# Performance work log

Hardware: AMD Instinct MI355X
Metric: run time of the kernel (lower is better)

## Reference

```python
import jax, jax.numpy as jnp
import numpy as np

MAX_OOV = 50

def setup_inputs() -> dict:
    key = jax.random.key(0)
    ks = jax.random.split(key, 20)
    B, T, Tc, E, H, V = 128, 256, 200, 256, 512, 50000
    s = 0.02
    inp = {
        'input': jax.random.randint(ks[0], (B, 1), 0, V),
        'h0': jax.random.normal(ks[1], (1, B, H), jnp.float32),
        'c0': jax.random.normal(ks[2], (1, B, H), jnp.float32),
        'encoder_outputs': jax.random.normal(ks[3], (B, T, H), jnp.float32),
        'context_encoder_outputs': jax.random.normal(ks[4], (B, Tc, H), jnp.float32),
        'context_input': jax.random.randint(ks[5], (B, Tc), 0, V + MAX_OOV),
        'embedding': jax.random.normal(ks[6], (V, E), jnp.float32) * s,
        'W_ih': jax.random.normal(ks[7], (4 * H, E), jnp.float32) * s,
        'W_hh': jax.random.normal(ks[8], (4 * H, H), jnp.float32) * s,
        'b_ih': jnp.zeros((4 * H,), jnp.float32),
        'b_hh': jnp.zeros((4 * H,), jnp.float32),
        'attn_W': jax.random.normal(ks[9], (H, H), jnp.float32) * s,
        'attn_b': jnp.zeros((H,), jnp.float32),
        'cattn_W': jax.random.normal(ks[10], (H, H), jnp.float32) * s,
        'cattn_b': jnp.zeros((H,), jnp.float32),
        'gen_W': jax.random.normal(ks[11], (1, 3 * H + E), jnp.float32) * s,
        'gen_b': jnp.zeros((1,), jnp.float32),
        'sig_b': jax.random.uniform(ks[12], (1,), jnp.float32, -0.1, 0.1),
        'out_W': jax.random.normal(ks[13], (V, H), jnp.float32) * s,
        'out_b': jnp.zeros((V,), jnp.float32),
    }
    return inp

def reference(input, h0, c0, encoder_outputs, context_encoder_outputs, context_input,
              embedding, W_ih, W_hh, b_ih, b_hh, attn_W, attn_b, cattn_W, cattn_b,
              gen_W, gen_b, sig_b, out_W, out_b):
    B = input.shape[0]
    V = out_W.shape[0]
    Vext = V + MAX_OOV
    # embedding lookup (input_len == 1)
    emb = embedding[input[:, 0]]                       # [B, E]
    # single-step LSTM (PyTorch gate order: i, f, g, o)
    gates = emb @ W_ih.T + b_ih + h0[0] @ W_hh.T + b_hh  # [B, 4H]
    i, f, g, o = jnp.split(gates, 4, axis=-1)
    c1 = jax.nn.sigmoid(f) * c0[0] + jax.nn.sigmoid(i) * jnp.tanh(g)
    h1 = jax.nn.sigmoid(o) * jnp.tanh(c1)              # [B, H]
    output = h1
    # attention over encoder_outputs (context_only)
    dec = output @ attn_W.T + attn_b                   # [B, H]
    scores = jax.nn.softmax(jnp.einsum('bth,bh->bt', encoder_outputs, dec), axis=1)
    context = jnp.einsum('bt,bth->bh', scores, encoder_outputs)
    # context attention (score_only)
    cdec = output @ cattn_W.T + cattn_b
    cscores = jax.nn.softmax(jnp.einsum('bth,bh->bt', context_encoder_outputs, cdec), axis=1)  # [B, Tc]
    cctx = jnp.einsum('bt,bth->bh', cscores, context_encoder_outputs)
    # generation probability
    feats = jnp.concatenate([context, cctx, output, emb], axis=1)  # [B, 3H+E]
    p_gen = jax.nn.sigmoid(feats @ gen_W.T + gen_b + sig_b)        # [B, 1]
    ctx_len = (context_input > 0).sum(axis=1, keepdims=True)
    p_gen = jnp.where(ctx_len == 0, jnp.float32(1.0), p_gen)
    # vocab distribution, extended with oov zeros
    p_vocab = jax.nn.softmax(output @ out_W.T + out_b, axis=1)
    p_vocab = jnp.concatenate([p_vocab, jnp.zeros((B, MAX_OOV), p_vocab.dtype)], axis=1)
    # copy distribution: scatter-add attention scores into extended vocab
    p_copy = jnp.zeros((B, Vext), p_vocab.dtype).at[
        jnp.arange(B)[:, None], context_input].add(cscores)
    prob = p_gen * p_vocab + (1.0 - p_gen) * p_copy
    logp = jnp.log(jnp.clip(prob, 1e-10))
    return logp, (h1[None], c1[None])
```

## Files before the change

### kernel.cpp

```cpp
#include <hip/hip_runtime.h>
#include <hip/hip_bf16.h>

#define BB 128
#define T_ENC 256
#define T_CTX 200
#define E_DIM 256
#define H_DIM 512
#define V_DIM 50000
#define N_OOV 50
#define VEXT  50050
#define FOURH 2048
#define K_GATES 768
#define LOGP_SZ (BB * VEXT)
#define OUT_H1_OFF LOGP_SZ
#define OUT_C1_OFF (LOGP_SZ + BB * H_DIM)
#define VCHUNK 2048
#define NCHUNK 25
#define NBIG 782

typedef __bf16 bf16x8 __attribute__((ext_vector_type(8)));
typedef float  floatx4 __attribute__((ext_vector_type(4)));

__device__ __forceinline__ float wave_sum(float v) {
#pragma unroll
  for (int m = 32; m > 0; m >>= 1) v += __shfl_xor(v, m, 64);
  return v;
}

__device__ __forceinline__ float sigm(float x) { return 1.0f / (1.0f + __expf(-x)); }

__device__ __forceinline__ unsigned f2bf2(float a, float b) {
  unsigned ua = __float_as_uint(a), ub = __float_as_uint(b);
  ua = (ua + 0x7FFFu + ((ua >> 16) & 1u)) >> 16;
  ub = (ub + 0x7FFFu + ((ub >> 16) & 1u)) & 0xFFFF0000u;
  return ua | ub;
}

__global__ __launch_bounds__(256) void prep_all(
    const float* __restrict__ W_ih, const float* __restrict__ W_hh,
    const float* __restrict__ attnW, const float* __restrict__ cattnW,
    const float* __restrict__ attnb, const float* __restrict__ cattnb,
    const int* __restrict__ input, const float* __restrict__ embT,
    const float* __restrict__ h0,
    __bf16* __restrict__ Wcat, __bf16* __restrict__ Wattn, float* __restrict__ attnbc,
    __bf16* __restrict__ Abuf, float* __restrict__ embf) {
  int n = blockIdx.x, tid = threadIdx.x;
  if (n < 2048) {
    unsigned* wr = (unsigned*)(Wcat + (size_t)n * K_GATES);
    for (int idx = tid; idx < 384; idx += 256) {
      int e0 = idx * 2;
      float2 x = (e0 < 256) ? *(const float2*)(W_ih + (size_t)n * E_DIM + e0)
                            : *(const float2*)(W_hh + (size_t)n * H_DIM + e0 - 256);
      wr[idx] = f2bf2(x.x, x.y);
    }
    if (n < 1024) {
      const float* src = (n < 512) ? (attnW + (size_t)n * H_DIM) : (cattnW + (size_t)(n - 512) * H_DIM);
      unsigned* wa = (unsigned*)(Wattn + (size_t)n * H_DIM);
      float2 x = *(const float2*)(src + tid * 2);
      wa[tid] = f2bf2(x.x, x.y);
    }
    if (n < 4) {
      int i = n * 256 + tid;
      attnbc[i] = (i < 512) ? attnb[i] : cattnb[i - 512];
    }
  } else {
    int b = n - 2048;
    int tok = input[b];
    unsigned* ar = (unsigned*)(Abuf + (size_t)b * K_GATES);
    for (int idx = tid; idx < 384; idx += 256) {
      int e0 = idx * 2;
      float2 x;
      if (e0 < 256) {
        x = *(const float2*)(embT + (size_t)tok * E_DIM + e0);
        *(float2*)(embf + b * E_DIM + e0) = x;
      } else {
        x = *(const float2*)(h0 + (size_t)b * H_DIM + e0 - 256);
      }
      ar[idx] = f2bf2(x.x, x.y);
    }
  }
}

template <int BF32>
__device__ __forceinline__ void gemm64_body(
    const __bf16* __restrict__ Abf, const void* __restrict__ Bsrc,
    const float* __restrict__ bias, float* __restrict__ C,
    int n0, int N, int Koff, int Klen, int Kpitch, int ldc) {
  __shared__ __bf16 As[128][72];
  __shared__ __bf16 Bs[64][72];
  int tid = threadIdx.x, lane = tid & 63, wid = tid >> 6;

  floatx4 acc[2][4];
#pragma unroll
  for (int i = 0; i < 2; i++)
#pragma unroll
    for (int j = 0; j < 4; j++) acc[i][j] = (floatx4){0.f, 0.f, 0.f, 0.f};

  int arow = tid >> 1, ahalf = tid & 1;
  int brow = tid >> 2, bq = tid & 3;
  int gnb = n0 + brow; if (gnb > N - 1) gnb = N - 1;

  const __bf16* abase = Abf + (size_t)arow * Kpitch + Koff + ahalf * 32;
  const float*  bfb = (const float*)Bsrc + (size_t)gnb * Kpitch + Koff + bq * 16;
  const __bf16* bhb = (const __bf16*)Bsrc + (size_t)gnb * Kpitch + Koff + bq * 16;

  uint4 ra[4];
  float4 rbf[4];
  uint4 rbh[2];
  {
    const uint4* s = (const uint4*)abase;
    ra[0] = s[0]; ra[1] = s[1]; ra[2] = s[2]; ra[3] = s[3];
    if (BF32) { const float4* t = (const float4*)bfb; rbf[0] = t[0]; rbf[1] = t[1]; rbf[2] = t[2]; rbf[3] = t[3]; }
    else      { const uint4* t = (const uint4*)bhb;  rbh[0] = t[0]; rbh[1] = t[1]; }
  }

  for (int k0 = 0; k0 < Klen; k0 += 64) {
    __syncthreads();
    { uint4* d = (uint4*)&As[arow][ahalf * 32]; d[0] = ra[0]; d[1] = ra[1]; d[2] = ra[2]; d[3] = ra[3]; }
    if (BF32) {
      uint4 o0, o1;
      o0.x = f2bf2(rbf[0].x, rbf[0].y); o0.y = f2bf2(rbf[0].z, rbf[0].w);
      o0.z = f2bf2(rbf[1].x, rbf[1].y); o0.w = f2bf2(rbf[1].z, rbf[1].w);
      o1.x = f2bf2(rbf[2].x, rbf[2].y); o1.y = f2bf2(rbf[2].z, rbf[2].w);
      o1.z = f2bf2(rbf[3].x, rbf[3].y); o1.w = f2bf2(rbf[3].z, rbf[3].w);
      uint4* d = (uint4*)&Bs[brow][bq * 16]; d[0] = o0; d[1] = o1;
    } else {
      uint4* d = (uint4*)&Bs[brow][bq * 16]; d[0] = rbh[0]; d[1] = rbh[1];
    }
    if (k0 + 64 < Klen) {
      const uint4* s = (const uint4*)(abase + k0 + 64);
      ra[0] = s[0]; ra[1] = s[1]; ra[2] = s[2]; ra[3] = s[3];
      if (BF32) { const float4* t = (const float4*)(bfb + k0 + 64); rbf[0] = t[0]; rbf[1] = t[1]; rbf[2] = t[2]; rbf[3] = t[3]; }
      else      { const uint4* t = (const uint4*)(bhb + k0 + 64);  rbh[0] = t[0]; rbh[1] = t[1]; }
    }
    __syncthreads();
#pragma unroll
    for (int kk = 0; kk < 64; kk += 32) {
      int kbase = kk + (lane >> 4) * 8;
      bf16x8 a0 = *(const bf16x8*)&As[wid * 32 + (lane & 15)][kbase];
      bf16x8 a1 = *(const bf16x8*)&As[wid * 32 + 16 + (lane & 15)][kbase];
      bf16x8 bfr[4];
#pragma unroll
      for (int j = 0; j < 4; j++) bfr[j] = *(const bf16x8*)&Bs[j * 16 + (lane & 15)][kbase];
#pragma unroll
      for (int j = 0; j < 4; j++) {
        acc[0][j] = __builtin_amdgcn_mfma_f32_16x16x32_bf16(a0, bfr[j], acc[0][j], 0, 0, 0);
        acc[1][j] = __builtin_amdgcn_mfma_f32_16x16x32_bf16(a1, bfr[j], acc[1][j], 0, 0, 0);
      }
    }
  }
  int cn = lane & 15, cq = lane >> 4;
#pragma unroll
  for (int i = 0; i < 2; i++)
#pragma unroll
    for (int j = 0; j < 4; j++)
#pragma unroll
      for (int r = 0; r < 4; r++) {
        int row = wid * 32 + i * 16 + cq * 4 + r;
        int col = n0 + j * 16 + cn;
        if (col < N) {
          float v = acc[i][j][r];
          if (bias) v += bias[col];
          C[(size_t)row * ldc + col] = v;
        }
      }
}

__global__ __launch_bounds__(256) void gates_gemm(
    const __bf16* __restrict__ Abuf, const __bf16* __restrict__ Wcat,
    float* __restrict__ g0, float* __restrict__ g1) {
  int bx = blockIdx.x;
  int kh = bx >> 5, nb = bx & 31;
  gemm64_body<0>(Abuf, Wcat, nullptr, kh ? g1 : g0, nb * 64, FOURH, kh * 384, 384, K_GATES, FOURH);
}

__global__ __launch_bounds__(256) void mega_gemm(
    const __bf16* __restrict__ h1b, const float* __restrict__ outW,
    const float* __restrict__ outb, float* __restrict__ Cbig,
    const __bf16* __restrict__ Wattn, const float* __restrict__ attnbc,
    float* __restrict__ decbuf) {
  int bx = blockIdx.x;
  if (bx < NBIG) gemm64_body<1>(h1b, outW, outb, Cbig, bx * 64, V_DIM, 0, H_DIM, H_DIM, VEXT);
  else           gemm64_body<0>(h1b, Wattn, attnbc, decbuf, (bx - NBIG) * 64, 1024, 0, H_DIM, H_DIM, 1024);
}

__global__ __launch_bounds__(256) void lstm_kernel(
    const float* __restrict__ gA, const float* __restrict__ gB,
    const float* __restrict__ b_ih, const float* __restrict__ b_hh,
    const float* __restrict__ c0,
    float* __restrict__ h1_out, float* __restrict__ c1_out, __bf16* __restrict__ h1b) {
  int idx = blockIdx.x * 256 + threadIdx.x;
  int b = idx >> 9, j = idx & 511;
  const float* ga = gA + b * FOURH;
  const float* gb = gB + b * FOURH;
  float iv = ga[j]        + gb[j]        + b_ih[j]        + b_hh[j];
  float fv = ga[512 + j]  + gb[512 + j]  + b_ih[512 + j]  + b_hh[512 + j];
  float gv = ga[1024 + j] + gb[1024 + j] + b_ih[1024 + j] + b_hh[1024 + j];
  float ov = ga[1536 + j] + gb[1536 + j] + b_ih[1536 + j] + b_hh[1536 + j];
  float c1 = sigm(fv) * c0[idx] + sigm(iv) * tanhf(gv);
  float h1 = sigm(ov) * tanhf(c1);
  h1_out[idx] = h1;
  c1_out[idx] = c1;
  h1b[idx] = (__bf16)h1;
}

__device__ __forceinline__ void flash_body(
    int g, const float* __restrict__ enc, const float* __restrict__ cenc,
    const float* __restrict__ decbuf, float* __restrict__ opart,
    float2* __restrict__ mlb, float* __restrict__ rawsc) {
  __shared__ float so[4][512];
  __shared__ float sml[4][2];
  int b = g & 127;
  int cc = g >> 7;
  int which = cc >> 2, chunk = cc & 3;
  int tchunk = which ? 50 : 64;
  int t0 = chunk * tchunk;
  const float* src = which ? (cenc + (size_t)b * T_CTX * H_DIM) : (enc + (size_t)b * T_ENC * H_DIM);
  const float* decp = decbuf + b * 1024 + which * 512;
  int tid = threadIdx.x, lane = tid & 63, wid = tid >> 6;
  float4 d0 = *(const float4*)(decp + lane * 8);
  float4 d1 = *(const float4*)(decp + lane * 8 + 4);
  float m = -1e30f, l = 0.f;
  float4 o0 = {0.f, 0.f, 0.f, 0.f}, o1 = {0.f, 0.f, 0.f, 0.f};
  for (int t = t0 + wid; t < t0 + tchunk; t += 4) {
    const float* row = src + (size_t)t * H_DIM + lane * 8;
    float4 r0 = *(const float4*)row;
    float4 r1 = *(const float4*)(row + 4);
    float p = r0.x * d0.x + r0.y * d0.y + r0.z * d0.z + r0.w * d0.w +
              r1.x * d1.x + r1.y * d1.y + r1.z * d1.z + r1.w * d1.w;
    p = wave_sum(p);
    if (which && lane == 0) rawsc[b * T_CTX + t] = p;
    float mn = fmaxf(m, p);
    float sc = __expf(m - mn);
    float e  = __expf(p - mn);
    l = l * sc + e;
    o0.x = o0.x * sc + e * r0.x; o0.y = o0.y * sc + e * r0.y;
    o0.z = o0.z * sc + e * r0.z; o0.w = o0.w * sc + e * r0.w;
    o1.x = o1.x * sc + e * r1.x; o1.y = o1.y * sc + e * r1.y;
    o1.z = o1.z * sc + e * r1.z; o1.w = o1.w * sc + e * r1.w;
    m = mn;
  }
  *(float4*)&so[wid][lane * 8]     = o0;
  *(float4*)&so[wid][lane * 8 + 4] = o1;
  if (lane == 0) { sml[wid][0] = m; sml[wid][1] = l; }
  __syncthreads();
  float M = fmaxf(fmaxf(sml[0][0], sml[1][0]), fmaxf(sml[2][0], sml[3][0]));
  float w0 = __expf(sml[0][0] - M), w1 = __expf(sml[1][0] - M);
  float w2 = __expf(sml[2][0] - M), w3 = __expf(sml[3][0] - M);
  float L = w0 * sml[0][1] + w1 * sml[1][1] + w2 * sml[2][1] + w3 * sml[3][1];
  int h = tid, h2 = tid + 256;
  float O0 = w0 * so[0][h]  + w1 * so[1][h]  + w2 * so[2][h]  + w3 * so[3][h];
  float O1 = w0 * so[0][h2] + w1 * so[1][h2] + w2 * so[2][h2] + w3 * so[3][h2];
  opart[(size_t)g * 512 + h]  = O0;
  opart[(size_t)g * 512 + h2] = O1;
  if (tid == 0) mlb[g] = make_float2(M, L);
}

__device__ __forceinline__ void stats_body(
    int bx, const float* __restrict__ logits,
    float* __restrict__ mpart, float* __restrict__ spart) {
  __shared__ float sm[256], ss[256];
  int b = bx & 127, c = bx >> 7;
  int tid = threadIdx.x;
  const float* rowp = logits + (size_t)b * VEXT;
  int v0 = c * VCHUNK + tid * 8;
  float m = -1e30f, s = 0.f;
#pragma unroll
  for (int k = 0; k < 4; k++) {
    int v = v0 + 2 * k;
    float2 x = *(const float2*)(rowp + v);
    if (v < V_DIM) {
      float xv = x.x;
      if (xv > m) { s = s * __expf(m - xv) + 1.0f; m = xv; } else s += __expf(xv - m);
    }
    if (v + 1 < V_DIM) {
      float xv = x.y;
      if (xv > m) { s = s * __expf(m - xv) + 1.0f; m = xv; } else s += __expf(xv - m);
    }
  }
  sm[tid] = m; ss[tid] = s; __syncthreads();
  for (int st = 128; st; st >>= 1) {
    if (tid < st) {
      float m2 = sm[tid + st], s2 = ss[tid + st];
      float mo = fmaxf(sm[tid], m2);
      ss[tid] = ss[tid] * __expf(sm[tid] - mo) + s2 * __expf(m2 - mo);
      sm[tid] = mo;
    }
    __syncthreads();
  }
  if (tid == 0) { mpart[bx] = sm[0]; spart[bx] = ss[0]; }
}

__global__ __launch_bounds__(256) void fs_kernel(
    const float* __restrict__ logits, float* __restrict__ mpart, float* __restrict__ spart,
    const float* __restrict__ enc, const float* __restrict__ cenc,
    const float* __restrict__ decbuf, float* __restrict__ opart,
    float2* __restrict__ mlb, float* __restrict__ rawsc) {
  int bx = blockIdx.x;
  if (bx < NCHUNK * 128) stats_body(bx, logits, mpart, spart);
  else flash_body(bx - NCHUNK * 128, enc, cenc, decbuf, opart, mlb, rawsc);
}

__global__ __launch_bounds__(256) void comb_kernel(
    const float* __restrict__ opart, const float2* __restrict__ mlb,
    float* __restrict__ ctx, float* __restrict__ cctx,
    float* __restrict__ Mc, float* __restrict__ Lc,
    const float* __restrict__ mpart, const float* __restrict__ spart,
    float* __restrict__ rowm, float* __restrict__ rows_) {
  int bw = blockIdx.x;
  int tid = threadIdx.x;
  if (bw < 256) {
    int b = bw & 127, which = bw >> 7;
    int g0 = (which * 4) * 128 + b;
    float2 ml0 = mlb[g0], ml1 = mlb[g0 + 128], ml2 = mlb[g0 + 256], ml3 = mlb[g0 + 384];
    float M = fmaxf(fmaxf(ml0.x, ml1.x), fmaxf(ml2.x, ml3.x));
    float w0 = __expf(ml0.x - M), w1 = __expf(ml1.x - M);
    float w2 = __expf(ml2.x - M), w3 = __expf(ml3.x - M);
    float L = w0 * ml0.y + w1 * ml1.y + w2 * ml2.y + w3 * ml3.y;
    float invL = 1.0f / L;
    float s0 = w0 * opart[(size_t)g0 * 512 + tid]         + w1 * opart[(size_t)(g0 + 128) * 512 + tid] +
               w2 * opart[(size_t)(g0 + 256) * 512 + tid] + w3 * opart[(size_t)(g0 + 384) * 512 + tid];
    int t2 = tid + 256;
    float s1 = w0 * opart[(size_t)g0 * 512 + t2]          + w1 * opart[(size_t)(g0 + 128) * 512 + t2] +
               w2 * opart[(size_t)(g0 + 256) * 512 + t2]  + w3 * opart[(size_t)(g0 + 384) * 512 + t2];
    float* outp = (which ? cctx : ctx) + b * 512;
    outp[tid] = s0 * invL;
    outp[t2]  = s1 * invL;
    if (which && tid == 0) { Mc[b] = M; Lc[b] = L; }
  } else if (tid < 128) {
    int b = tid;
    float m = -1e30f, s = 0.f;
#pragma unroll
    for (int c = 0; c < NCHUNK; c++) {
      float m2 = mpart[c * 128 + b], s2 = spart[c * 128 + b];
      float mo = fmaxf(m, m2);
      s = s * __expf(m - mo) + s2 * __expf(m2 - mo);
      m = mo;
    }
    rowm[b] = m; rows_[b] = s;
  }
}

__global__ __launch_bounds__(256) void final_kernel(
    float* __restrict__ out, const int* __restrict__ ctx_inp,
    const float* __restrict__ rawsc, const float* __restrict__ Mc, const float* __restrict__ Lc,
    const float* __restrict__ rowm, const float* __restrict__ rows_,
    const float* __restrict__ ctx, const float* __restrict__ cctx,
    const float* __restrict__ h1f, const float* __restrict__ embf,
    const float* __restrict__ genW, const float* __restrict__ genb,
    const float* __restrict__ sigb) {
  __shared__ float pc[VCHUNK];
  __shared__ float red8[8];
  int bx = blockIdx.x;
  int b = bx & 127, c = bx >> 7;
  int tid = threadIdx.x, lane = tid & 63, wid = tid >> 6;
  int cidx = (tid < T_CTX) ? ctx_inp[b * T_CTX + tid] : 0;
  float acc = 0.f;
  for (int j = tid; j < 1792; j += 256) {
    float x;
    if (j < 512) x = ctx[b * 512 + j];
    else if (j < 1024) x = cctx[b * 512 + j - 512];
    else if (j < 1536) x = h1f[b * 512 + j - 1024];
    else x = embf[b * 256 + j - 1536];
    acc += x * genW[j];
  }
  float cnt = (tid < T_CTX && cidx > 0) ? 1.f : 0.f;
  acc = wave_sum(acc); cnt = wave_sum(cnt);
  if (lane == 0) { red8[wid] = acc; red8[4 + wid] = cnt; }
#pragma unroll
  for (int k = 0; k < 8; k++) pc[tid * 8 + k] = 0.f;
  __syncthreads();
  float pg;
  {
    float a = red8[0] + red8[1] + red8[2] + red8[3];
    float cn = red8[4] + red8[5] + red8[6] + red8[7];
    pg = sigm(a + genb[0] + sigb[0]);
    if (cn == 0.f) pg = 1.0f;
  }
  int v0c = c * VCHUNK;
  if (tid < T_CTX) {
    int rel = cidx - v0c;
    if (rel >= 0 && rel < VCHUNK) {
      float val = __expf(rawsc[b * T_CTX + tid] - Mc[b]) / Lc[b];
      atomicAdd(&pc[rel], val);
    }
  }
  __syncthreads();
  float m = rowm[b], inv = 1.0f / rows_[b], pc1 = 1.0f - pg;
  float* rowp = out + (size_t)b * VEXT;
  int li0 = tid * 8;
#pragma unroll
  for (int k = 0; k < 4; k++) {
    int li = li0 + 2 * k;
    int v = v0c + li;
    float2 x = *(const float2*)(rowp + v);
    float pv0 = (v < V_DIM)     ? __expf(x.x - m) * inv : 0.f;
    float pv1 = (v + 1 < V_DIM) ? __expf(x.y - m) * inv : 0.f;
    float r0 = __logf(fmaxf(pg * pv0 + pc1 * pc[li],     1e-10f));
    float r1 = __logf(fmaxf(pg * pv1 + pc1 * pc[li + 1], 1e-10f));
    if (v + 1 < VEXT)      *(float2*)(rowp + v) = make_float2(r0, r1);
    else if (v < VEXT)     rowp[v] = r0;
  }
}

extern "C" void kernel_launch(void* const* d_in, const int* in_sizes, int n_in,
                              void* d_out, int out_size, void* d_ws, size_t ws_size,
                              hipStream_t stream) {
  const int*   input   = (const int*)d_in[0];
  const float* h0      = (const float*)d_in[1];
  const float* c0      = (const float*)d_in[2];
  const float* enc     = (const float*)d_in[3];
  const float* cenc    = (const float*)d_in[4];
  const int*   ctx_inp = (const int*)d_in[5];
  const float* embT    = (const float*)d_in[6];
  const float* W_ih    = (const float*)d_in[7];
  const float* W_hh    = (const float*)d_in[8];
  const float* b_ih    = (const float*)d_in[9];
  const float* b_hh    = (const float*)d_in[10];
  const float* attnW   = (const float*)d_in[11];
  const float* attnb   = (const float*)d_in[12];
  const float* cattnW  = (const float*)d_in[13];
  const float* cattnb  = (const float*)d_in[14];
  const float* genW    = (const float*)d_in[15];
  const float* genb    = (const float*)d_in[16];
  const float* sigb    = (const float*)d_in[17];
  const float* outW    = (const float*)d_in[18];
  const float* outb    = (const float*)d_in[19];

  char* ws = (char*)d_ws;
  __bf16* Wcat   = (__bf16*)(ws + 0);
  __bf16* Wattn  = (__bf16*)(ws + 3145728);
  float*  attnbc = (float*)(ws + 4194304);
  __bf16* Abuf   = (__bf16*)(ws + 4198400);
  float*  embf   = (float*)(ws + 4395008);
  float*  gates  = (float*)(ws + 4526080);
  float*  gates2 = (float*)(ws + 5574656);
  __bf16* h1b    = (__bf16*)(ws + 6623232);
  float*  decbuf = (float*)(ws + 6754304);
  float*  opart  = (float*)(ws + 7278592);
  float2* mlb    = (float2*)(ws + 9375744);
  float*  ctx    = (float*)(ws + 9383936);
  float*  cctx   = (float*)(ws + 9646080);
  float*  rawsc  = (float*)(ws + 9908224);
  float*  Mc     = (float*)(ws + 10010624);
  float*  Lc     = (float*)(ws + 10011136);
  float*  mpart  = (float*)(ws + 10011648);
  float*  spart  = (float*)(ws + 10024448);
  float*  rowm   = (float*)(ws + 10037248);
  float*  rows_  = (float*)(ws + 10037760);

  float* outF = (float*)d_out;
  float* h1_out = outF + OUT_H1_OFF;
  float* c1_out = outF + OUT_C1_OFF;

  prep_all<<<2176, 256, 0, stream>>>(W_ih, W_hh, attnW, cattnW, attnb, cattnb,
                                     input, embT, h0, Wcat, Wattn, attnbc, Abuf, embf);
  gates_gemm<<<64, 256, 0, stream>>>(Abuf, Wcat, gates, gates2);
  lstm_kernel<<<256, 256, 0, stream>>>(gates, gates2, b_ih, b_hh, c0, h1_out, c1_out, h1b);
  mega_gemm<<<NBIG + 16, 256, 0, stream>>>(h1b, outW, outb, outF, Wattn, attnbc, decbuf);
  fs_kernel<<<NCHUNK * 128 + 1024, 256, 0, stream>>>(outF, mpart, spart,
                                                     enc, cenc, decbuf, opart, mlb, rawsc);
  comb_kernel<<<257, 256, 0, stream>>>(opart, mlb, ctx, cctx, Mc, Lc, mpart, spart, rowm, rows_);
  final_kernel<<<NCHUNK * 128, 256, 0, stream>>>(outF, ctx_inp, rawsc, Mc, Lc, rowm, rows_,
                                                 ctx, cctx, h1_out, embf, genW, genb, sigb);
}
```

Measured before the change: 392.5 us.

## Fuse softmax row stats into vocab GEMM epilogue and drop stats/combine kernels

The vocab GEMM epilogue now computes per-64-column max and sum-exp partials for each row, so the separate pass that re-read the whole 128x50000 logits matrix to get softmax statistics is gone. The attention-partial combine is folded into the final kernel, which removes comb_kernel and one launch. Logits go to a padded workspace buffer when space allows, and the final kernel reads from there and writes to the output. In exchange the final kernel merges 782 partials per row and redoes the attention combine in every chunk block.

```diff
diff --git a/kernel.cpp b/kernel.cpp
--- a/kernel.cpp
+++ b/kernel.cpp
@@ -17,6 +17,7 @@
 #define VCHUNK 2048
 #define NCHUNK 25
 #define NBIG 782
+#define MSP_PITCH 784
 
 typedef __bf16 bf16x8 __attribute__((ext_vector_type(8)));
 typedef float  floatx4 __attribute__((ext_vector_type(4)));
@@ -81,13 +82,13 @@
   }
 }
 
-template <int BF32>
+template <int BF32, int STATS>
 __device__ __forceinline__ void gemm64_body(
+    __bf16 (* __restrict__ As)[72], __bf16 (* __restrict__ Bs)[72],
     const __bf16* __restrict__ Abf, const void* __restrict__ Bsrc,
     const float* __restrict__ bias, float* __restrict__ C,
-    int n0, int N, int Koff, int Klen, int Kpitch, int ldc) {
-  __shared__ __bf16 As[128][72];
-  __shared__ __bf16 Bs[64][72];
+    int n0, int N, int Koff, int Klen, int Kpitch, size_t ldc,
+    float2* __restrict__ mspart, int cb) {
   int tid = threadIdx.x, lane = tid & 63, wid = tid >> 6;
 
   floatx4 acc[2][4];
@@ -164,24 +165,57 @@
           C[(size_t)row * ldc + col] = v;
         }
       }
+  if (STATS) {
+#pragma unroll
+    for (int i = 0; i < 2; i++)
+#pragma unroll
+      for (int r = 0; r < 4; r++) {
+        int row = wid * 32 + i * 16 + cq * 4 + r;
+        float v[4]; float mx = -1e30f;
+#pragma unroll
+        for (int j = 0; j < 4; j++) {
+          int col = n0 + j * 16 + cn;
+          float x = acc[i][j][r] + bias[col < N ? col : N - 1];
+          v[j] = (col < N) ? x : -1e30f;
+          mx = fmaxf(mx, v[j]);
+        }
+#pragma unroll
+        for (int mk = 1; mk <= 8; mk <<= 1) mx = fmaxf(mx, __shfl_xor(mx, mk, 64));
+        float s = 0.f;
+#pragma unroll
+        for (int j = 0; j < 4; j++) s += (v[j] > -1e29f) ? __expf(v[j] - mx) : 0.f;
+#pragma unroll
+        for (int mk = 1; mk <= 8; mk <<= 1) s += __shfl_xor(s, mk, 64);
+        if (cn == 0) mspart[(size_t)row * MSP_PITCH + cb] = make_float2(mx, s);
+      }
+  }
 }
 
 __global__ __launch_bounds__(256) void gates_gemm(
     const __bf16* __restrict__ Abuf, const __bf16* __restrict__ Wcat,
     float* __restrict__ g0, float* __restrict__ g1) {
+  __shared__ __bf16 As[128][72];
+  __shared__ __bf16 Bs[64][72];
   int bx = blockIdx.x;
   int kh = bx >> 5, nb = bx & 31;
-  gemm64_body<0>(Abuf, Wcat, nullptr, kh ? g1 : g0, nb * 64, FOURH, kh * 384, 384, K_GATES, FOURH);
+  gemm64_body<0, 0>(As, Bs, Abuf, Wcat, nullptr, kh ? g1 : g0, nb * 64, FOURH,
+                    kh * 384, 384, K_GATES, FOURH, nullptr, 0);
 }
 
 __global__ __launch_bounds__(256) void mega_gemm(
     const __bf16* __restrict__ h1b, const float* __restrict__ outW,
-    const float* __restrict__ outb, float* __restrict__ Cbig,
+    const float* __restrict__ outb, float* __restrict__ logits, size_t lpitch,
     const __bf16* __restrict__ Wattn, const float* __restrict__ attnbc,
-    float* __restrict__ decbuf) {
+    float* __restrict__ decbuf, float2* __restrict__ mspart) {
+  __shared__ __bf16 As[128][72];
+  __shared__ __bf16 Bs[64][72];
   int bx = blockIdx.x;
-  if (bx < NBIG) gemm64_body<1>(h1b, outW, outb, Cbig, bx * 64, V_DIM, 0, H_DIM, H_DIM, VEXT);
-  else           gemm64_body<0>(h1b, Wattn, attnbc, decbuf, (bx - NBIG) * 64, 1024, 0, H_DIM, H_DIM, 1024);
+  if (bx < NBIG)
+    gemm64_body<1, 1>(As, Bs, h1b, outW, outb, logits, bx * 64, V_DIM,
+                      0, H_DIM, H_DIM, lpitch, mspart, bx);
+  else
+    gemm64_body<0, 0>(As, Bs, h1b, Wattn, attnbc, decbuf, (bx - NBIG) * 64, 1024,
+                      0, H_DIM, H_DIM, 1024, nullptr, 0);
 }
 
 __global__ __launch_bounds__(256) void lstm_kernel(
@@ -204,12 +238,13 @@
   h1b[idx] = (__bf16)h1;
 }
 
-__device__ __forceinline__ void flash_body(
-    int g, const float* __restrict__ enc, const float* __restrict__ cenc,
+__global__ __launch_bounds__(256) void flash_kernel(
+    const float* __restrict__ enc, const float* __restrict__ cenc,
     const float* __restrict__ decbuf, float* __restrict__ opart,
     float2* __restrict__ mlb, float* __restrict__ rawsc) {
   __shared__ float so[4][512];
   __shared__ float sml[4][2];
+  int g = blockIdx.x;
   int b = g & 127;
   int cc = g >> 7;
   int which = cc >> 2, chunk = cc & 3;
@@ -256,29 +291,60 @@
   if (tid == 0) mlb[g] = make_float2(M, L);
 }
 
-__device__ __forceinline__ void stats_body(
-    int bx, const float* __restrict__ logits,
-    float* __restrict__ mpart, float* __restrict__ spart) {
+__global__ __launch_bounds__(256) void final_kernel(
+    const float* __restrict__ logits, size_t lpitch,
+    float* __restrict__ out, const int* __restrict__ ctx_inp,
+    const float* __restrict__ rawsc, const float2* __restrict__ mlb,
+    const float2* __restrict__ mspart, const float* __restrict__ opart,
+    const float* __restrict__ h1f, const float* __restrict__ embf,
+    const float* __restrict__ genW, const float* __restrict__ genb,
+    const float* __restrict__ sigb) {
+  __shared__ float pc[VCHUNK];
   __shared__ float sm[256], ss[256];
+  __shared__ float red8[8];
+  int bx = blockIdx.x;
   int b = bx & 127, c = bx >> 7;
-  int tid = threadIdx.x;
-  const float* rowp = logits + (size_t)b * VEXT;
-  int v0 = c * VCHUNK + tid * 8;
+  int tid = threadIdx.x, lane = tid & 63, wid = tid >> 6;
+  int cidx = (tid < T_CTX) ? ctx_inp[b * T_CTX + tid] : 0;
+
+  float2 e0 = mlb[b], e1 = mlb[128 + b], e2 = mlb[256 + b], e3 = mlb[384 + b];
+  float2 f0 = mlb[512 + b], f1 = mlb[640 + b], f2 = mlb[768 + b], f3 = mlb[896 + b];
+  float M0 = fmaxf(fmaxf(e0.x, e1.x), fmaxf(e2.x, e3.x));
+  float a0 = __expf(e0.x - M0), a1 = __expf(e1.x - M0), a2 = __expf(e2.x - M0), a3 = __expf(e3.x - M0);
+  float L0 = a0 * e0.y + a1 * e1.y + a2 * e2.y + a3 * e3.y;
+  float M1 = fmaxf(fmaxf(f0.x, f1.x), fmaxf(f2.x, f3.x));
+  float c0_ = __expf(f0.x - M1), c1_ = __expf(f1.x - M1), c2_ = __expf(f2.x - M1), c3_ = __expf(f3.x - M1);
+  float L1 = c0_ * f0.y + c1_ * f1.y + c2_ * f2.y + c3_ * f3.y;
+
+  float acc = 0.f;
+  for (int j = tid; j < 1792; j += 256) {
+    float x;
+    if (j < 1024) {
+      int which = j >> 9, h = j & 511;
+      const float* op = opart + ((size_t)(which * 512 + b) * 512) + h;
+      if (which == 0)
+        x = (a0 * op[0] + a1 * op[128 * 512] + a2 * op[256 * 512] + a3 * op[384 * 512]) / L0;
+      else
+        x = (c0_ * op[0] + c1_ * op[128 * 512] + c2_ * op[256 * 512] + c3_ * op[384 * 512]) / L1;
+    } else if (j < 1536) x = h1f[b * 512 + j - 1024];
+    else x = embf[b * 256 + j - 1536];
+    acc += x * genW[j];
+  }
+  float cnt = (tid < T_CTX && cidx > 0) ? 1.f : 0.f;
+  acc = wave_sum(acc); cnt = wave_sum(cnt);
+  if (lane == 0) { red8[wid] = acc; red8[4 + wid] = cnt; }
+
   float m = -1e30f, s = 0.f;
-#pragma unroll
-  for (int k = 0; k < 4; k++) {
-    int v = v0 + 2 * k;
-    float2 x = *(const float2*)(rowp + v);
-    if (v < V_DIM) {
-      float xv = x.x;
-      if (xv > m) { s = s * __expf(m - xv) + 1.0f; m = xv; } else s += __expf(xv - m);
-    }
-    if (v + 1 < V_DIM) {
-      float xv = x.y;
-      if (xv > m) { s = s * __expf(m - xv) + 1.0f; m = xv; } else s += __expf(xv - m);
-    }
-  }
-  sm[tid] = m; ss[tid] = s; __syncthreads();
+  for (int cb = tid; cb < NBIG; cb += 256) {
+    float2 p = mspart[(size_t)b * MSP_PITCH + cb];
+    float mo = fmaxf(m, p.x);
+    s = s * __expf(m - mo) + p.y * __expf(p.x - mo);
+    m = mo;
+  }
+  sm[tid] = m; ss[tid] = s;
+#pragma unroll
+  for (int k = 0; k < 8; k++) pc[tid * 8 + k] = 0.f;
+  __syncthreads();
   for (int st = 128; st; st >>= 1) {
     if (tid < st) {
       float m2 = sm[tid + st], s2 = ss[tid + st];
@@ -288,88 +354,7 @@
     }
     __syncthreads();
   }
-  if (tid == 0) { mpart[bx] = sm[0]; spart[bx] = ss[0]; }
-}
-
-__global__ __launch_bounds__(256) void fs_kernel(
-    const float* __restrict__ logits, float* __restrict__ mpart, float* __restrict__ spart,
-    const float* __restrict__ enc, const float* __restrict__ cenc,
-    const float* __restrict__ decbuf, float* __restrict__ opart,
-    float2* __restrict__ mlb, float* __restrict__ rawsc) {
-  int bx = blockIdx.x;
-  if (bx < NCHUNK * 128) stats_body(bx, logits, mpart, spart);
-  else flash_body(bx - NCHUNK * 128, enc, cenc, decbuf, opart, mlb, rawsc);
-}
-
-__global__ __launch_bounds__(256) void comb_kernel(
-    const float* __restrict__ opart, const float2* __restrict__ mlb,
-    float* __restrict__ ctx, float* __restrict__ cctx,
-    float* __restrict__ Mc, float* __restrict__ Lc,
-    const float* __restrict__ mpart, const float* __restrict__ spart,
-    float* __restrict__ rowm, float* __restrict__ rows_) {
-  int bw = blockIdx.x;
-  int tid = threadIdx.x;
-  if (bw < 256) {
-    int b = bw & 127, which = bw >> 7;
-    int g0 = (which * 4) * 128 + b;
-    float2 ml0 = mlb[g0], ml1 = mlb[g0 + 128], ml2 = mlb[g0 + 256], ml3 = mlb[g0 + 384];
-    float M = fmaxf(fmaxf(ml0.x, ml1.x), fmaxf(ml2.x, ml3.x));
-    float w0 = __expf(ml0.x - M), w1 = __expf(ml1.x - M);
-    float w2 = __expf(ml2.x - M), w3 = __expf(ml3.x - M);
-    float L = w0 * ml0.y + w1 * ml1.y + w2 * ml2.y + w3 * ml3.y;
-    float invL = 1.0f / L;
-    float s0 = w0 * opart[(size_t)g0 * 512 + tid]         + w1 * opart[(size_t)(g0 + 128) * 512 + tid] +
-               w2 * opart[(size_t)(g0 + 256) * 512 + tid] + w3 * opart[(size_t)(g0 + 384) * 512 + tid];
-    int t2 = tid + 256;
-    float s1 = w0 * opart[(size_t)g0 * 512 + t2]          + w1 * opart[(size_t)(g0 + 128) * 512 + t2] +
-               w2 * opart[(size_t)(g0 + 256) * 512 + t2]  + w3 * opart[(size_t)(g0 + 384) * 512 + t2];
-    float* outp = (which ? cctx : ctx) + b * 512;
-    outp[tid] = s0 * invL;
-    outp[t2]  = s1 * invL;
-    if (which && tid == 0) { Mc[b] = M; Lc[b] = L; }
-  } else if (tid < 128) {
-    int b = tid;
-    float m = -1e30f, s = 0.f;
-#pragma unroll
-    for (int c = 0; c < NCHUNK; c++) {
-      float m2 = mpart[c * 128 + b], s2 = spart[c * 128 + b];
-      float mo = fmaxf(m, m2);
-      s = s * __expf(m - mo) + s2 * __expf(m2 - mo);
-      m = mo;
-    }
-    rowm[b] = m; rows_[b] = s;
-  }
-}
-
-__global__ __launch_bounds__(256) void final_kernel(
-    float* __restrict__ out, const int* __restrict__ ctx_inp,
-    const float* __restrict__ rawsc, const float* __restrict__ Mc, const float* __restrict__ Lc,
-    const float* __restrict__ rowm, const float* __restrict__ rows_,
-    const float* __restrict__ ctx, const float* __restrict__ cctx,
-    const float* __restrict__ h1f, const float* __restrict__ embf,
-    const float* __restrict__ genW, const float* __restrict__ genb,
-    const float* __restrict__ sigb) {
-  __shared__ float pc[VCHUNK];
-  __shared__ float red8[8];
-  int bx = blockIdx.x;
-  int b = bx & 127, c = bx >> 7;
-  int tid = threadIdx.x, lane = tid & 63, wid = tid >> 6;
-  int cidx = (tid < T_CTX) ? ctx_inp[b * T_CTX + tid] : 0;
-  float acc = 0.f;
-  for (int j = tid; j < 1792; j += 256) {
-    float x;
-    if (j < 512) x = ctx[b * 512 + j];
-    else if (j < 1024) x = cctx[b * 512 + j - 512];
-    else if (j < 1536) x = h1f[b * 512 + j - 1024];
-    else x = embf[b * 256 + j - 1536];
-    acc += x * genW[j];
-  }
-  float cnt = (tid < T_CTX && cidx > 0) ? 1.f : 0.f;
-  acc = wave_sum(acc); cnt = wave_sum(cnt);
-  if (lane == 0) { red8[wid] = acc; red8[4 + wid] = cnt; }
-#pragma unroll
-  for (int k = 0; k < 8; k++) pc[tid * 8 + k] = 0.f;
-  __syncthreads();
+  float rm = sm[0], rs = ss[0];
   float pg;
   {
     float a = red8[0] + red8[1] + red8[2] + red8[3];
@@ -381,25 +366,26 @@
   if (tid < T_CTX) {
     int rel = cidx - v0c;
     if (rel >= 0 && rel < VCHUNK) {
-      float val = __expf(rawsc[b * T_CTX + tid] - Mc[b]) / Lc[b];
+      float val = __expf(rawsc[b * T_CTX + tid] - M1) / L1;
       atomicAdd(&pc[rel], val);
     }
   }
   __syncthreads();
-  float m = rowm[b], inv = 1.0f / rows_[b], pc1 = 1.0f - pg;
-  float* rowp = out + (size_t)b * VEXT;
+  float inv = 1.0f / rs, pc1 = 1.0f - pg;
+  const float* rowsrc = logits + (size_t)b * lpitch;
+  float* rowdst = out + (size_t)b * VEXT;
   int li0 = tid * 8;
 #pragma unroll
   for (int k = 0; k < 4; k++) {
     int li = li0 + 2 * k;
     int v = v0c + li;
-    float2 x = *(const float2*)(rowp + v);
-    float pv0 = (v < V_DIM)     ? __expf(x.x - m) * inv : 0.f;
-    float pv1 = (v + 1 < V_DIM) ? __expf(x.y - m) * inv : 0.f;
+    float2 x = *(const float2*)(rowsrc + v);
+    float pv0 = (v < V_DIM)     ? __expf(x.x - rm) * inv : 0.f;
+    float pv1 = (v + 1 < V_DIM) ? __expf(x.y - rm) * inv : 0.f;
     float r0 = __logf(fmaxf(pg * pv0 + pc1 * pc[li],     1e-10f));
     float r1 = __logf(fmaxf(pg * pv1 + pc1 * pc[li + 1], 1e-10f));
-    if (v + 1 < VEXT)      *(float2*)(rowp + v) = make_float2(r0, r1);
-    else if (v < VEXT)     rowp[v] = r0;
+    if (v + 1 < VEXT)      *(float2*)(rowdst + v) = make_float2(r0, r1);
+    else if (v < VEXT)     rowdst[v] = r0;
   }
 }
 
@@ -439,17 +425,16 @@
   float*  decbuf = (float*)(ws + 6754304);
   float*  opart  = (float*)(ws + 7278592);
   float2* mlb    = (float2*)(ws + 9375744);
-  float*  ctx    = (float*)(ws + 9383936);
-  float*  cctx   = (float*)(ws + 9646080);
-  float*  rawsc  = (float*)(ws + 9908224);
-  float*  Mc     = (float*)(ws + 10010624);
-  float*  Lc     = (float*)(ws + 10011136);
-  float*  mpart  = (float*)(ws + 10011648);
-  float*  spart  = (float*)(ws + 10024448);
-  float*  rowm   = (float*)(ws + 10037248);
-  float*  rows_  = (float*)(ws + 10037760);
+  float*  rawsc  = (float*)(ws + 9383936);
+  float2* mspart = (float2*)(ws + 9486336);
+  const size_t logits_off = 10289152;
+  const size_t LPITCH_AL = 50176;
 
   float* outF = (float*)d_out;
+  bool padded = ws_size >= logits_off + (size_t)BB * LPITCH_AL * 4;
+  float* logits = padded ? (float*)(ws + logits_off) : outF;
+  size_t lpitch = padded ? LPITCH_AL : (size_t)VEXT;
+
   float* h1_out = outF + OUT_H1_OFF;
   float* c1_out = outF + OUT_C1_OFF;
 
@@ -457,10 +442,9 @@
                                      input, embT, h0, Wcat, Wattn, attnbc, Abuf, embf);
   gates_gemm<<<64, 256, 0, stream>>>(Abuf, Wcat, gates, gates2);
   lstm_kernel<<<256, 256, 0, stream>>>(gates, gates2, b_ih, b_hh, c0, h1_out, c1_out, h1b);
-  mega_gemm<<<NBIG + 16, 256, 0, stream>>>(h1b, outW, outb, outF, Wattn, attnbc, decbuf);
-  fs_kernel<<<NCHUNK * 128 + 1024, 256, 0, stream>>>(outF, mpart, spart,
-                                                     enc, cenc, decbuf, opart, mlb, rawsc);
-  comb_kernel<<<257, 256, 0, stream>>>(opart, mlb, ctx, cctx, Mc, Lc, mpart, spart, rowm, rows_);
-  final_kernel<<<NCHUNK * 128, 256, 0, stream>>>(outF, ctx_inp, rawsc, Mc, Lc, rowm, rows_,
-                                                 ctx, cctx, h1_out, embf, genW, genb, sigb);
-}
+  mega_gemm<<<NBIG + 16, 256, 0, stream>>>(h1b, outW, outb, logits, lpitch,
+                                           Wattn, attnbc, decbuf, mspart);
+  flash_kernel<<<1024, 256, 0, stream>>>(enc, cenc, decbuf, opart, mlb, rawsc);
+  final_kernel<<<NCHUNK * 128, 256, 0, stream>>>(logits, lpitch, outF, ctx_inp, rawsc, mlb,
+                                                 mspart, opart, h1_out, embf, genW, genb, sigb);
+}
```

New measurement: 392.1 us. Within noise of the previous version (-0.1%).
